# Kernel tuning notes

Measured on AMD Instinct MI355X. Metric: run time of the kernel, lower is better.

The kernel has to match this reference:

```python
import jax, jax.numpy as jnp
import numpy as np

T, B = 256, 512
IMG_FLAT = 25          # 5*5*num_channels
FEAT = 16; LOC = 4; EMB = 4
LSTM_IN = FEAT + LOC + EMB  # 24
H = 128
GRID = 10.0


def _lin(k, out_d, in_d, scale=0.05):
    kw, kb = jax.random.split(k)
    return (jax.random.normal(kw, (out_d, in_d), jnp.float32) * scale,
            jax.random.normal(kb, (out_d,), jnp.float32) * scale)


def setup_inputs() -> dict:
    key = jax.random.key(0)
    ks = jax.random.split(key, 16)
    image = jax.random.uniform(ks[0], (T * B, 5, 5), jnp.float32) * 255.0
    location = jax.random.uniform(ks[1], (T * B, 2), jnp.float32) * GRID
    message = jax.random.normal(ks[2], (T * B, 1), jnp.float32)
    done = jax.random.randint(ks[3], (T * B,), 0, 2, jnp.int32)
    h0 = jnp.zeros((1, B, H), jnp.float32)
    c0 = jnp.zeros((1, B, H), jnp.float32)
    Wv1, bv1 = _lin(ks[4], 256, IMG_FLAT)
    Wv2, bv2 = _lin(ks[5], 256, 256)
    Wv3, bv3 = _lin(ks[6], 128, 256)
    Wv4, bv4 = _lin(ks[7], FEAT, 128)
    Wl, bl = _lin(ks[8], LOC, 2)
    Wm, bm = _lin(ks[9], EMB, 1)
    Wih, bih = _lin(ks[10], 4 * H, LSTM_IN)
    Whh, bhh = _lin(ks[11], 4 * H, H)
    return dict(image=image, location=location, message=message, done=done,
                h0=h0, c0=c0,
                Wv1=Wv1, bv1=bv1, Wv2=Wv2, bv2=bv2, Wv3=Wv3, bv3=bv3,
                Wv4=Wv4, bv4=bv4, Wl=Wl, bl=bl, Wm=Wm, bm=bm,
                Wih=Wih, bih=bih, Whh=Whh, bhh=bhh)


def _get_states(image, location, message, done_f, h0, c0,
                Wv1, bv1, Wv2, bv2, Wv3, bv3, Wv4, bv4,
                Wl, bl, Wm, bm, Wih, bih, Whh, bhh):
    batch = h0.shape[1]
    # encoders (all rows at once, faithful to torch version)
    x = image.reshape(image.shape[0], -1) / 255.0
    f = jax.nn.relu(x @ Wv1.T + bv1)
    f = jax.nn.relu(f @ Wv2.T + bv2)
    f = jax.nn.relu(f @ Wv3.T + bv3)
    image_feat = jax.nn.relu(f @ Wv4.T + bv4)                  # [TB, 16]
    loc_feat = (location / GRID) @ Wl.T + bl                    # [TB, 4]
    msg = (1.0 - done_f)[:, None] * message
    msg_feat = jax.nn.relu(msg @ Wm.T + bm)                     # [TB, 4]
    hid = jnp.concatenate([image_feat, loc_feat, msg_feat], axis=1)
    hid = hid.reshape(-1, batch, LSTM_IN)                       # [T, B, 24]
    d_seq = done_f.reshape(-1, batch)                           # [T, B]

    def step(carry, xd):
        h, c = carry
        x_t, d_t = xd
        mask = (1.0 - d_t)[:, None]
        h = h * mask
        c = c * mask
        gates = x_t @ Wih.T + bih + h @ Whh.T + bhh             # [B, 4H]
        i, fg, g, o = jnp.split(gates, 4, axis=-1)
        c = jax.nn.sigmoid(fg) * c + jax.nn.sigmoid(i) * jnp.tanh(g)
        h = jax.nn.sigmoid(o) * jnp.tanh(c)
        return (h, c), h

    (hT, cT), hs = jax.lax.scan(step, (h0[0], c0[0]), (hid, d_seq))
    new_hidden = hs.reshape(-1, H)                              # [TB, 128]
    return new_hidden, hT[None], cT[None]


def reference(image, location, message, done, h0, c0,
              Wv1, bv1, Wv2, bv2, Wv3, bv3, Wv4, bv4,
              Wl, bl, Wm, bm, Wih, bih, Whh, bhh):
    done_f = done.astype(jnp.float32)
    return _get_states(image, location, message, done_f, h0, c0,
                       Wv1, bv1, Wv2, bv2, Wv3, bv3, Wv4, bv4,
                       Wl, bl, Wm, bm, Wih, bih, Whh, bhh)
```

## Files before the change

### kernel.cpp

```cpp
#include <hip/hip_runtime.h>
#include <hip/hip_bf16.h>

#define T_STEPS 256
#define BATCH   512
#define HID     128
#define TBROWS  (T_STEPS * BATCH)
#define XH_STRIDE 32

typedef short  bh8   __attribute__((ext_vector_type(8)));
typedef _Float16 h8  __attribute__((ext_vector_type(8)));
typedef float  f32x4 __attribute__((ext_vector_type(4)));

__device__ __forceinline__ unsigned short f2bf_bits(float x) {
    union { float f; unsigned int u; } a; a.f = x;
    unsigned int r = a.u + 0x7fffu + ((a.u >> 16) & 1u);
    return (unsigned short)(r >> 16);
}
__device__ __forceinline__ unsigned short f2h_bits(float x) {
    union { _Float16 h; unsigned short u; } z; z.h = (_Float16)x; return z.u;
}
__device__ __forceinline__ unsigned int pack2h(float a, float b) {
    union { _Float16 h[2]; unsigned int u; } z;
    z.h[0] = (_Float16)a; z.h[1] = (_Float16)b; return z.u;
}
__device__ __forceinline__ unsigned int pack2bf(float a, float b) {
    return (unsigned int)f2bf_bits(a) | ((unsigned int)f2bf_bits(b) << 16);
}

#if __has_builtin(__builtin_amdgcn_rcpf)
__device__ __forceinline__ float frcp(float x) { return __builtin_amdgcn_rcpf(x); }
#else
__device__ __forceinline__ float frcp(float x) { return 1.0f / x; }
#endif
#if __has_builtin(__builtin_amdgcn_exp2f)
__device__ __forceinline__ float fexp2(float x) { return __builtin_amdgcn_exp2f(x); }
#else
__device__ __forceinline__ float fexp2(float x) { return __expf(x * 0.6931471806f); }
#endif
#define LOG2E 1.442695041f
__device__ __forceinline__ float sigf(float x) {
    return frcp(1.0f + fexp2(-x * LOG2E));
}
__device__ __forceinline__ float tanh_fast(float x) {
    return fmaf(-2.0f, frcp(1.0f + fexp2(x * (2.0f * LOG2E))), 1.0f);
}

__device__ __forceinline__ void fragstore(unsigned short* dst, const float* W,
                                          int i, int NT, int Kreal) {
    const int j    = i & 7;
    const int lane = (i >> 3) & 63;
    const int ts   = i >> 9;
    const int nt   = ts % NT;
    const int ks   = ts / NT;
    const int n = nt * 16 + (lane & 15);
    const int k = ks * 32 + (lane >> 4) * 8 + j;
    dst[i] = (k < Kreal) ? f2bf_bits(W[n * Kreal + k]) : (unsigned short)0;
}

#define NE1 8192
#define NE2 65536
#define NE3 32768
#define NE4 2048
#define NWC 81920
#define NBS 512
#define PREP_TOTAL (NE1 + NE2 + NE3 + NE4 + NWC + NBS)

__global__ __launch_bounds__(256) void prep_kernel(
    const float* __restrict__ W1, const float* __restrict__ W2,
    const float* __restrict__ W3, const float* __restrict__ W4,
    const float* __restrict__ Wih, const float* __restrict__ bih,
    const float* __restrict__ Whh, const float* __restrict__ bhh,
    unsigned short* __restrict__ w1f, unsigned short* __restrict__ w2f,
    unsigned short* __restrict__ w3f, unsigned short* __restrict__ w4f,
    unsigned short* __restrict__ wcf, float* __restrict__ bsum)
{
    int i = blockIdx.x * 256 + threadIdx.x;
    if (i < NE1) { fragstore(w1f, W1, i, 16, 25); return; }
    i -= NE1;
    if (i < NE2) { fragstore(w2f, W2, i, 16, 256); return; }
    i -= NE2;
    if (i < NE3) { fragstore(w3f, W3, i, 8, 256); return; }
    i -= NE3;
    if (i < NE4) { fragstore(w4f, W4, i, 1, 128); return; }
    i -= NE4;
    if (i < NWC) {
        const int j    = i & 7;
        const int lane = (i >> 3) & 63;
        const int ts   = i >> 9;
        const int mt   = ts / 5;
        const int kt   = ts - mt * 5;
        const int m = mt * 16 + (lane & 15);
        const int k = kt * 32 + (lane >> 4) * 8 + j;
        float v = 0.0f;
        if (k < 128)      v = Whh[m * 128 + k];
        else if (k < 152) v = Wih[m * 24 + (k - 128)];
        wcf[i] = f2h_bits(v);
        return;
    }
    i -= NWC;
    if (i < NBS) bsum[i] = bih[i] + bhh[i];
}

#define ASTRIDE 264

__global__ __launch_bounds__(256) void encoder_kernel(
    const float* __restrict__ img,
    const float* __restrict__ loc,
    const float* __restrict__ msg,
    const int*   __restrict__ done,
    const float* __restrict__ B1, const float* __restrict__ B2,
    const float* __restrict__ B3, const float* __restrict__ B4,
    const float* __restrict__ Wl, const float* __restrict__ Bl,
    const float* __restrict__ Wm, const float* __restrict__ Bm,
    const unsigned short* __restrict__ w1f, const unsigned short* __restrict__ w2f,
    const unsigned short* __restrict__ w3f, const unsigned short* __restrict__ w4f,
    unsigned short* __restrict__ xcat_h)
{
    __shared__ __align__(16) unsigned short actA[4][32][ASTRIDE];
    __shared__ __align__(16) unsigned short actB[4][32][ASTRIDE];

    const int tid  = threadIdx.x;
    const int w    = tid >> 6;
    const int lane = tid & 63;
    const int n    = lane & 15;
    const int quad = lane >> 4;
    const int wrow0 = blockIdx.x * 128 + w * 32;

    if (tid < 128) {
        const int grow = blockIdx.x * 128 + tid;
        const float l0 = loc[(size_t)grow * 2 + 0] * 0.1f;
        const float l1 = loc[(size_t)grow * 2 + 1] * 0.1f;
        #pragma unroll
        for (int c = 0; c < 4; ++c)
            xcat_h[(size_t)grow * XH_STRIDE + 16 + c] =
                f2h_bits(fmaf(Wl[c * 2 + 0], l0, fmaf(Wl[c * 2 + 1], l1, Bl[c])));
        const float mm = (1.0f - (float)done[grow]) * msg[grow];
        #pragma unroll
        for (int c = 0; c < 4; ++c)
            xcat_h[(size_t)grow * XH_STRIDE + 20 + c] =
                f2h_bits(fmaxf(fmaf(Wm[c], mm, Bm[c]), 0.0f));
    }

    const f32x4 zero4 = {0.0f, 0.0f, 0.0f, 0.0f};

    {
        bh8 bimg[2];
        #pragma unroll
        for (int sg = 0; sg < 2; ++sg) {
            const size_t grow = wrow0 + sg * 16 + n;
            #pragma unroll
            for (int j = 0; j < 8; ++j) {
                const int k = quad * 8 + j;
                const float v = (k < 25) ? img[grow * 25 + k] * (1.0f / 255.0f) : 0.0f;
                bimg[sg][j] = (short)f2bf_bits(v);
            }
        }
        f32x4 a1[16][2];
        #pragma unroll
        for (int mt = 0; mt < 16; ++mt) {
            const bh8 a = *reinterpret_cast<const bh8*>(w1f + (size_t)(mt * 64 + lane) * 8);
            a1[mt][0] = __builtin_amdgcn_mfma_f32_16x16x32_bf16(a, bimg[0], zero4, 0, 0, 0);
            a1[mt][1] = __builtin_amdgcn_mfma_f32_16x16x32_bf16(a, bimg[1], zero4, 0, 0, 0);
        }
        #pragma unroll
        for (int mt = 0; mt < 16; ++mt) {
            const float4 bv = *reinterpret_cast<const float4*>(B1 + mt * 16 + quad * 4);
            #pragma unroll
            for (int sg = 0; sg < 2; ++sg) {
                const float v0 = fmaxf(a1[mt][sg][0] + bv.x, 0.0f);
                const float v1 = fmaxf(a1[mt][sg][1] + bv.y, 0.0f);
                const float v2 = fmaxf(a1[mt][sg][2] + bv.z, 0.0f);
                const float v3 = fmaxf(a1[mt][sg][3] + bv.w, 0.0f);
                uint2 pk; pk.x = pack2bf(v0, v1); pk.y = pack2bf(v2, v3);
                *reinterpret_cast<uint2*>(&actA[w][sg * 16 + n][mt * 16 + quad * 4]) = pk;
            }
        }
    }
    __syncthreads();

    {
        f32x4 a2[16][2];
        #pragma unroll
        for (int mt = 0; mt < 16; ++mt) { a2[mt][0] = zero4; a2[mt][1] = zero4; }
        #pragma unroll
        for (int kt = 0; kt < 8; ++kt) {
            const bh8 b0 = *reinterpret_cast<const bh8*>(&actA[w][n][kt * 32 + quad * 8]);
            const bh8 b1 = *reinterpret_cast<const bh8*>(&actA[w][16 + n][kt * 32 + quad * 8]);
            #pragma unroll
            for (int mt = 0; mt < 16; ++mt) {
                const bh8 a = *reinterpret_cast<const bh8*>(
                    w2f + (size_t)((kt * 16 + mt) * 64 + lane) * 8);
                a2[mt][0] = __builtin_amdgcn_mfma_f32_16x16x32_bf16(a, b0, a2[mt][0], 0, 0, 0);
                a2[mt][1] = __builtin_amdgcn_mfma_f32_16x16x32_bf16(a, b1, a2[mt][1], 0, 0, 0);
            }
        }
        #pragma unroll
        for (int mt = 0; mt < 16; ++mt) {
            const float4 bv = *reinterpret_cast<const float4*>(B2 + mt * 16 + quad * 4);
            #pragma unroll
            for (int sg = 0; sg < 2; ++sg) {
                const float v0 = fmaxf(a2[mt][sg][0] + bv.x, 0.0f);
                const float v1 = fmaxf(a2[mt][sg][1] + bv.y, 0.0f);
                const float v2 = fmaxf(a2[mt][sg][2] + bv.z, 0.0f);
                const float v3 = fmaxf(a2[mt][sg][3] + bv.w, 0.0f);
                uint2 pk; pk.x = pack2bf(v0, v1); pk.y = pack2bf(v2, v3);
                *reinterpret_cast<uint2*>(&actB[w][sg * 16 + n][mt * 16 + quad * 4]) = pk;
            }
        }
    }
    __syncthreads();

    {
        f32x4 a3[8][2];
        #pragma unroll
        for (int mt = 0; mt < 8; ++mt) { a3[mt][0] = zero4; a3[mt][1] = zero4; }
        #pragma unroll
        for (int kt = 0; kt < 8; ++kt) {
            const bh8 b0 = *reinterpret_cast<const bh8*>(&actB[w][n][kt * 32 + quad * 8]);
            const bh8 b1 = *reinterpret_cast<const bh8*>(&actB[w][16 + n][kt * 32 + quad * 8]);
            #pragma unroll
            for (int mt = 0; mt < 8; ++mt) {
                const bh8 a = *reinterpret_cast<const bh8*>(
                    w3f + (size_t)((kt * 8 + mt) * 64 + lane) * 8);
                a3[mt][0] = __builtin_amdgcn_mfma_f32_16x16x32_bf16(a, b0, a3[mt][0], 0, 0, 0);
                a3[mt][1] = __builtin_amdgcn_mfma_f32_16x16x32_bf16(a, b1, a3[mt][1], 0, 0, 0);
            }
        }
        #pragma unroll
        for (int mt = 0; mt < 8; ++mt) {
            const float4 bv = *reinterpret_cast<const float4*>(B3 + mt * 16 + quad * 4);
            #pragma unroll
            for (int sg = 0; sg < 2; ++sg) {
                const float v0 = fmaxf(a3[mt][sg][0] + bv.x, 0.0f);
                const float v1 = fmaxf(a3[mt][sg][1] + bv.y, 0.0f);
                const float v2 = fmaxf(a3[mt][sg][2] + bv.z, 0.0f);
                const float v3 = fmaxf(a3[mt][sg][3] + bv.w, 0.0f);
                uint2 pk; pk.x = pack2bf(v0, v1); pk.y = pack2bf(v2, v3);
                *reinterpret_cast<uint2*>(&actA[w][sg * 16 + n][mt * 16 + quad * 4]) = pk;
            }
        }
    }
    __syncthreads();

    {
        f32x4 a4[2] = {zero4, zero4};
        #pragma unroll
        for (int kt = 0; kt < 4; ++kt) {
            const bh8 b0 = *reinterpret_cast<const bh8*>(&actA[w][n][kt * 32 + quad * 8]);
            const bh8 b1 = *reinterpret_cast<const bh8*>(&actA[w][16 + n][kt * 32 + quad * 8]);
            const bh8 a = *reinterpret_cast<const bh8*>(w4f + (size_t)(kt * 64 + lane) * 8);
            a4[0] = __builtin_amdgcn_mfma_f32_16x16x32_bf16(a, b0, a4[0], 0, 0, 0);
            a4[1] = __builtin_amdgcn_mfma_f32_16x16x32_bf16(a, b1, a4[1], 0, 0, 0);
        }
        const float4 bv = *reinterpret_cast<const float4*>(B4 + quad * 4);
        #pragma unroll
        for (int sg = 0; sg < 2; ++sg) {
            const int grow = wrow0 + sg * 16 + n;
            const float v0 = fmaxf(a4[sg][0] + bv.x, 0.0f);
            const float v1 = fmaxf(a4[sg][1] + bv.y, 0.0f);
            const float v2 = fmaxf(a4[sg][2] + bv.z, 0.0f);
            const float v3 = fmaxf(a4[sg][3] + bv.w, 0.0f);
            uint2 pk; pk.x = pack2h(v0, v1); pk.y = pack2h(v2, v3);
            *reinterpret_cast<uint2*>(xcat_h + (size_t)grow * XH_STRIDE + quad * 4) = pk;
        }
    }
}

#define COLS 2
#define HXS 168

__global__ __launch_bounds__(256) void lstm_kernel(
    const unsigned short* __restrict__ xcat_h,
    const int*   __restrict__ done,
    const float* __restrict__ h0,
    const float* __restrict__ c0,
    const unsigned short* __restrict__ wcf,
    const float* __restrict__ bsum,
    float* __restrict__ out)
{
    __shared__ __align__(16) unsigned short hx[2][16][HXS];
    __shared__ __align__(16) float gbuf[COLS][130][4];

    const int tid  = threadIdx.x;
    const int w    = tid >> 6;
    const int lane = tid & 63;
    const int n    = lane & 15;
    const int quad = lane >> 4;
    const int bb   = blockIdx.x * COLS;

    h8 wf[2][4][5];
    #pragma unroll
    for (int h = 0; h < 2; ++h)
        #pragma unroll
        for (int g = 0; g < 4; ++g)
            #pragma unroll
            for (int kt = 0; kt < 5; ++kt)
                wf[h][g][kt] = *reinterpret_cast<const h8*>(
                    wcf + (size_t)(((g * 8 + w + 4 * h) * 5 + kt) * 64 + lane) * 8);

    const int tn = tid >> 7;
    const int tu = tid & 127;
    float bi_t[4];
    #pragma unroll
    for (int g = 0; g < 4; ++g) bi_t[g] = bsum[g * 128 + tu];

    float c_ = c0[(size_t)(bb + tn) * HID + tu];
    const float h0v = h0[(size_t)(bb + tn) * HID + tu];

    for (int i = tid; i < 2 * 16 * HXS / 2; i += 256)
        reinterpret_cast<unsigned int*>(hx)[i] = 0u;
    __syncthreads();

    int mc = done[bb + tn];
    int mn = done[BATCH + bb + tn];
    hx[0][tn][tu] = f2h_bits(h0v * (1.0f - (float)mc));
    if (tid < COLS * 12) {
        const int nl = tid / 12, kp = tid - nl * 12;
        *reinterpret_cast<unsigned int*>(&hx[0][nl][128 + 2 * kp]) =
            *reinterpret_cast<const unsigned int*>(
                xcat_h + (size_t)(bb + nl) * XH_STRIDE + 2 * kp);
    }
    __syncthreads();

    float hl = 0.0f;

    #pragma unroll 1
    for (int s = 0; s < T_STEPS; ++s) {
        const int buf = s & 1;

        h8 bf[5];
        #pragma unroll
        for (int kt = 0; kt < 5; ++kt)
            bf[kt] = *reinterpret_cast<const h8*>(&hx[buf][n][kt * 32 + quad * 8]);

        unsigned int xreg = 0;
        if (tid < COLS * 12) {
            const int nl = tid / 12, kp = tid - nl * 12;
            const int rowx = (s + 1 < T_STEPS ? s + 1 : T_STEPS - 1) * BATCH + bb + nl;
            xreg = *reinterpret_cast<const unsigned int*>(
                xcat_h + (size_t)rowx * XH_STRIDE + 2 * kp);
        }
        const int mf = done[(s + 2 < T_STEPS ? s + 2 : T_STEPS - 1) * BATCH + bb + tn];

        f32x4 acc[2][4];
        #pragma unroll
        for (int h = 0; h < 2; ++h)
            #pragma unroll
            for (int g = 0; g < 4; ++g) acc[h][g] = (f32x4){0.0f, 0.0f, 0.0f, 0.0f};
        #pragma unroll
        for (int kt = 0; kt < 5; ++kt)
            #pragma unroll
            for (int h = 0; h < 2; ++h)
                #pragma unroll
                for (int g = 0; g < 4; ++g)
                    acc[h][g] = __builtin_amdgcn_mfma_f32_16x16x32_f16(
                        wf[h][g][kt], bf[kt], acc[h][g], 0, 0, 0);

        if (n < COLS) {
            #pragma unroll
            for (int h = 0; h < 2; ++h) {
                const int ub = (w + 4 * h) * 16 + quad * 4;
                #pragma unroll
                for (int r = 0; r < 4; ++r) {
                    float4 gv;
                    gv.x = acc[h][0][r]; gv.y = acc[h][1][r];
                    gv.z = acc[h][2][r]; gv.w = acc[h][3][r];
                    *reinterpret_cast<float4*>(&gbuf[n][ub + r][0]) = gv;
                }
            }
        }
        __syncthreads();

        const float4 gv = *reinterpret_cast<const float4*>(&gbuf[tn][tu][0]);
        const float mcur = 1.0f - (float)mc;
        const float mnxt = 1.0f - (float)mn;
        const float gi = gv.x + bi_t[0];
        const float gf = gv.y + bi_t[1];
        const float gg = gv.z + bi_t[2];
        const float go = gv.w + bi_t[3];
        const float cn = sigf(gf) * (c_ * mcur) + sigf(gi) * tanh_fast(gg);
        const float hn = sigf(go) * tanh_fast(cn);
        c_ = cn; hl = hn;

        const int row = s * BATCH + bb + tn;
        out[(size_t)row * HID + tu] = hn;
        hx[buf ^ 1][tn][tu] = f2h_bits(hn * mnxt);
        if (tid < COLS * 12) {
            const int nl = tid / 12, kp = tid - nl * 12;
            *reinterpret_cast<unsigned int*>(&hx[buf ^ 1][nl][128 + 2 * kp]) = xreg;
        }
        mc = mn; mn = mf;
        __syncthreads();
    }

    const size_t base = (size_t)TBROWS * HID;
    out[base + (size_t)(bb + tn) * HID + tu] = hl;
    out[base + (size_t)BATCH * HID + (size_t)(bb + tn) * HID + tu] = c_;
}

extern "C" void kernel_launch(void* const* d_in, const int* in_sizes, int n_in,
                              void* d_out, int out_size, void* d_ws, size_t ws_size,
                              hipStream_t stream) {
    const float* img  = (const float*)d_in[0];
    const float* loc  = (const float*)d_in[1];
    const float* msg  = (const float*)d_in[2];
    const int*   done = (const int*)d_in[3];
    const float* h0   = (const float*)d_in[4];
    const float* c0   = (const float*)d_in[5];
    const float* W1   = (const float*)d_in[6];
    const float* B1   = (const float*)d_in[7];
    const float* W2   = (const float*)d_in[8];
    const float* B2   = (const float*)d_in[9];
    const float* W3   = (const float*)d_in[10];
    const float* B3   = (const float*)d_in[11];
    const float* W4   = (const float*)d_in[12];
    const float* B4   = (const float*)d_in[13];
    const float* Wl   = (const float*)d_in[14];
    const float* Bl   = (const float*)d_in[15];
    const float* Wm   = (const float*)d_in[16];
    const float* Bm   = (const float*)d_in[17];
    const float* Wih  = (const float*)d_in[18];
    const float* bih  = (const float*)d_in[19];
    const float* Whh  = (const float*)d_in[20];
    const float* bhh  = (const float*)d_in[21];

    char* wsb = (char*)d_ws;
    unsigned short* xcat_h = (unsigned short*)wsb;
    unsigned short* w1f = (unsigned short*)(wsb + (size_t)TBROWS * XH_STRIDE * 2);
    unsigned short* w2f = w1f + NE1;
    unsigned short* w3f = w2f + NE2;
    unsigned short* w4f = w3f + NE3;
    unsigned short* wcf = w4f + NE4;
    float*          bsum = (float*)(wcf + NWC);

    float* out = (float*)d_out;

    prep_kernel<<<(PREP_TOTAL + 255) / 256, 256, 0, stream>>>(
        W1, W2, W3, W4, Wih, bih, Whh, bhh,
        w1f, w2f, w3f, w4f, wcf, bsum);
    encoder_kernel<<<TBROWS / 128, 256, 0, stream>>>(
        img, loc, msg, done, B1, B2, B3, B4, Wl, Bl, Wm, Bm,
        w1f, w2f, w3f, w4f, xcat_h);
    lstm_kernel<<<BATCH / COLS, 256, 0, stream>>>(
        xcat_h, done, h0, c0, wcf, bsum, out);
}
```

Before: 404.6 us.

## Split LSTM gate units across 8 waves and drop mid-step barrier

The LSTM kernel now runs 512 threads (8 waves), each wave owning 16 hidden units for all four gates. The cell update therefore reads gates from its own wave's scratch region, which removes the intra-step __syncthreads between the gate MMA and the cell update. Bias is folded into the accumulator init. It halves the MFMA chain per wave and the register weight footprint, but leaves half the lanes idle in the elementwise part. It also relies on intra-wave LDS ordering, with no explicit wave barrier between the scratch write and read.

```diff
diff --git a/kernel.cpp b/kernel.cpp
--- a/kernel.cpp
+++ b/kernel.cpp
@@ -269,7 +269,7 @@
 #define COLS 2
 #define HXS 168
 
-__global__ __launch_bounds__(256) void lstm_kernel(
+__global__ __launch_bounds__(512) void lstm_kernel(
     const unsigned short* __restrict__ xcat_h,
     const int*   __restrict__ done,
     const float* __restrict__ h0,
@@ -279,7 +279,7 @@
     float* __restrict__ out)
 {
     __shared__ __align__(16) unsigned short hx[2][16][HXS];
-    __shared__ __align__(16) float gbuf[COLS][130][4];
+    __shared__ __align__(16) float sc[8][COLS][16][4];
 
     const int tid  = threadIdx.x;
     const int w    = tid >> 6;
@@ -288,32 +288,39 @@
     const int quad = lane >> 4;
     const int bb   = blockIdx.x * COLS;
 
-    h8 wf[2][4][5];
+    h8 wf[4][5];
     #pragma unroll
-    for (int h = 0; h < 2; ++h)
-        #pragma unroll
-        for (int g = 0; g < 4; ++g)
-            #pragma unroll
-            for (int kt = 0; kt < 5; ++kt)
-                wf[h][g][kt] = *reinterpret_cast<const h8*>(
-                    wcf + (size_t)(((g * 8 + w + 4 * h) * 5 + kt) * 64 + lane) * 8);
-
-    const int tn = tid >> 7;
-    const int tu = tid & 127;
-    float bi_t[4];
+    for (int g = 0; g < 4; ++g)
+        #pragma unroll
+        for (int kt = 0; kt < 5; ++kt)
+            wf[g][kt] = *reinterpret_cast<const h8*>(
+                wcf + (size_t)(((g * 8 + w) * 5 + kt) * 64 + lane) * 8);
+
+    f32x4 bini[4];
     #pragma unroll
-    for (int g = 0; g < 4; ++g) bi_t[g] = bsum[g * 128 + tu];
-
-    float c_ = c0[(size_t)(bb + tn) * HID + tu];
-    const float h0v = h0[(size_t)(bb + tn) * HID + tu];
-
-    for (int i = tid; i < 2 * 16 * HXS / 2; i += 256)
+    for (int g = 0; g < 4; ++g) {
+        const float4 b = *reinterpret_cast<const float4*>(bsum + g * 128 + w * 16 + quad * 4);
+        bini[g] = (f32x4){b.x, b.y, b.z, b.w};
+    }
+
+    const int col   = quad & 1;
+    const int ul    = lane & 15;
+    const int unit  = w * 16 + ul;
+    const bool owner = lane < 32;
+
+    float c_ = 0.0f, h0v = 0.0f;
+    if (owner) {
+        c_  = c0[(size_t)(bb + col) * HID + unit];
+        h0v = h0[(size_t)(bb + col) * HID + unit];
+    }
+
+    for (int i = tid; i < 2 * 16 * HXS / 2; i += 512)
         reinterpret_cast<unsigned int*>(hx)[i] = 0u;
     __syncthreads();
 
-    int mc = done[bb + tn];
-    int mn = done[BATCH + bb + tn];
-    hx[0][tn][tu] = f2h_bits(h0v * (1.0f - (float)mc));
+    int mc = done[bb + col];
+    int mn = done[BATCH + bb + col];
+    if (owner) hx[0][col][unit] = f2h_bits(h0v * (1.0f - (float)mc));
     if (tid < COLS * 12) {
         const int nl = tid / 12, kp = tid - nl * 12;
         *reinterpret_cast<unsigned int*>(&hx[0][nl][128 + 2 * kp]) =
@@ -340,51 +347,38 @@
             xreg = *reinterpret_cast<const unsigned int*>(
                 xcat_h + (size_t)rowx * XH_STRIDE + 2 * kp);
         }
-        const int mf = done[(s + 2 < T_STEPS ? s + 2 : T_STEPS - 1) * BATCH + bb + tn];
-
-        f32x4 acc[2][4];
-        #pragma unroll
-        for (int h = 0; h < 2; ++h)
-            #pragma unroll
-            for (int g = 0; g < 4; ++g) acc[h][g] = (f32x4){0.0f, 0.0f, 0.0f, 0.0f};
+        const int mf = done[(s + 2 < T_STEPS ? s + 2 : T_STEPS - 1) * BATCH + bb + col];
+
+        f32x4 acc[4];
+        #pragma unroll
+        for (int g = 0; g < 4; ++g) acc[g] = bini[g];
         #pragma unroll
         for (int kt = 0; kt < 5; ++kt)
             #pragma unroll
-            for (int h = 0; h < 2; ++h)
-                #pragma unroll
-                for (int g = 0; g < 4; ++g)
-                    acc[h][g] = __builtin_amdgcn_mfma_f32_16x16x32_f16(
-                        wf[h][g][kt], bf[kt], acc[h][g], 0, 0, 0);
+            for (int g = 0; g < 4; ++g)
+                acc[g] = __builtin_amdgcn_mfma_f32_16x16x32_f16(
+                    wf[g][kt], bf[kt], acc[g], 0, 0, 0);
 
         if (n < COLS) {
             #pragma unroll
-            for (int h = 0; h < 2; ++h) {
-                const int ub = (w + 4 * h) * 16 + quad * 4;
-                #pragma unroll
-                for (int r = 0; r < 4; ++r) {
-                    float4 gv;
-                    gv.x = acc[h][0][r]; gv.y = acc[h][1][r];
-                    gv.z = acc[h][2][r]; gv.w = acc[h][3][r];
-                    *reinterpret_cast<float4*>(&gbuf[n][ub + r][0]) = gv;
-                }
-            }
-        }
-        __syncthreads();
-
-        const float4 gv = *reinterpret_cast<const float4*>(&gbuf[tn][tu][0]);
-        const float mcur = 1.0f - (float)mc;
-        const float mnxt = 1.0f - (float)mn;
-        const float gi = gv.x + bi_t[0];
-        const float gf = gv.y + bi_t[1];
-        const float gg = gv.z + bi_t[2];
-        const float go = gv.w + bi_t[3];
-        const float cn = sigf(gf) * (c_ * mcur) + sigf(gi) * tanh_fast(gg);
-        const float hn = sigf(go) * tanh_fast(cn);
-        c_ = cn; hl = hn;
-
-        const int row = s * BATCH + bb + tn;
-        out[(size_t)row * HID + tu] = hn;
-        hx[buf ^ 1][tn][tu] = f2h_bits(hn * mnxt);
+            for (int r = 0; r < 4; ++r) {
+                float4 gv;
+                gv.x = acc[0][r]; gv.y = acc[1][r];
+                gv.z = acc[2][r]; gv.w = acc[3][r];
+                *reinterpret_cast<float4*>(&sc[w][n][quad * 4 + r][0]) = gv;
+            }
+        }
+
+        if (owner) {
+            const float4 gv = *reinterpret_cast<const float4*>(&sc[w][col][ul][0]);
+            const float mcur = 1.0f - (float)mc;
+            const float mnxt = 1.0f - (float)mn;
+            const float cn = sigf(gv.y) * (c_ * mcur) + sigf(gv.x) * tanh_fast(gv.z);
+            const float hn = sigf(gv.w) * tanh_fast(cn);
+            c_ = cn; hl = hn;
+            out[(size_t)(s * BATCH + bb + col) * HID + unit] = hn;
+            hx[buf ^ 1][col][unit] = f2h_bits(hn * mnxt);
+        }
         if (tid < COLS * 12) {
             const int nl = tid / 12, kp = tid - nl * 12;
             *reinterpret_cast<unsigned int*>(&hx[buf ^ 1][nl][128 + 2 * kp]) = xreg;
@@ -394,8 +388,10 @@
     }
 
     const size_t base = (size_t)TBROWS * HID;
-    out[base + (size_t)(bb + tn) * HID + tu] = hl;
-    out[base + (size_t)BATCH * HID + (size_t)(bb + tn) * HID + tu] = c_;
+    if (owner) {
+        out[base + (size_t)(bb + col) * HID + unit] = hl;
+        out[base + (size_t)BATCH * HID + (size_t)(bb + col) * HID + unit] = c_;
+    }
 }
 
 extern "C" void kernel_launch(void* const* d_in, const int* in_sizes, int n_in,
@@ -441,6 +437,6 @@
     encoder_kernel<<<TBROWS / 128, 256, 0, stream>>>(
         img, loc, msg, done, B1, B2, B3, B4, Wl, Bl, Wm, Bm,
         w1f, w2f, w3f, w4f, xcat_h);
-    lstm_kernel<<<BATCH / COLS, 256, 0, stream>>>(
+    lstm_kernel<<<BATCH / COLS, 512, 0, stream>>>(
         xcat_h, done, h0, c0, wcf, bsum, out);
 }
```

Measured after the change: 373.1 us. -7.8%, faster.
